# Performance work log

Hardware: AMD Instinct MI355X
Metric: run time of the kernel (lower is better)

## Reference

```python
import math
import jax, jax.numpy as jnp
import numpy as np

N = 65536   # total nodes across episodes
H = 512     # hidden size
B = 4096    # number of episodes / decoding items
M = 32      # max neighbors (padded ragged valid_actions)


def setup_inputs() -> dict:
    key = jax.random.key(0)
    ks = jax.random.split(key, 9)
    s = 1.0 / math.sqrt(H)
    return {
        "h_static": jax.random.normal(ks[0], (N, H), jnp.float32),
        "h_dynamic": jax.random.normal(ks[1], (N, H), jnp.float32),
        "Ws_kvl": jax.random.normal(ks[2], (H, 3 * H), jnp.float32) * s,
        "Wd_kvl": jax.random.normal(ks[3], (H, 3 * H), jnp.float32) * s,
        "Wq": jax.random.normal(ks[4], (H, H), jnp.float32) * s,
        "batch": jax.random.randint(ks[5], (N,), 0, B, jnp.int32),
        "current_nodes": jax.random.randint(ks[6], (B,), 0, N),
        "neigh_idx": jax.random.randint(ks[7], (B, M), 0, N),
        "lengths": jax.random.randint(ks[8], (B,), 0, M + 1),
    }


def reference(h_static, h_dynamic, Ws_kvl, Wd_kvl, Wq, batch, current_nodes, neigh_idx, lengths):
    # precompute(): static KVL projection (full 3H GEMM then chunk, as in torch)
    kvl_s = h_static @ Ws_kvl            # [N, 3H]
    K_s = kvl_s[:, :H]
    # forward_batch(): dynamic projection
    kvl_d = h_dynamic @ Wd_kvl           # [N, 3H]
    K_d = kvl_d[:, :H]
    K = K_s + K_d                        # [N, H]  (V is computed but unused for outputs)
    q = (h_static[current_nodes] + h_dynamic[current_nodes]) @ Wq  # [B, H]

    # padded ragged neighbor attention (replaces the Python loop over B)
    Kn = K[neigh_idx]                                        # [B, M, H]
    compat = jnp.einsum('bmh,bh->bm', Kn, q) / math.sqrt(H)  # [B, M]
    mask = jnp.arange(M)[None, :] < lengths[:, None]         # [B, M]
    NEG = jnp.float32(-1e9)
    logits = jnp.where(mask, compat, NEG)

    # categorical sampling via Gumbel-max (Categorical(logits).sample())
    u = jax.random.uniform(jax.random.key(1), (B, M), jnp.float32, 1e-8, 1.0)
    g = -jnp.log(-jnp.log(u))
    idx = jnp.argmax(logits + g, axis=-1)                    # [B]

    logp = jax.nn.log_softmax(logits, axis=-1)               # [B, M]
    lp = jnp.take_along_axis(logp, idx[:, None], axis=1)[:, 0]
    actions = jnp.take_along_axis(neigh_idx, idx[:, None], axis=1)[:, 0]

    # empty neighbor list -> stay at current node, log_prob 0 (matches torch branch)
    nonempty = lengths > 0
    actions = jnp.where(nonempty, actions, current_nodes)
    lp = jnp.where(nonempty, lp, jnp.float32(0.0))
    return actions, lp
```

## Files before the change

kernel.cpp:

```cpp
#include <hip/hip_runtime.h>
#include <cstdint>
#include <cstddef>

#define HDIM 512
#define NM 32
#define NBATCH 4096
#define NNODE 65536
#define CAP 16

typedef float v4f __attribute__((ext_vector_type(4)));

__device__ __forceinline__ unsigned rotl32(unsigned x, unsigned d) {
  return (x << d) | (x >> (32u - d));
}

__device__ __forceinline__ void threefry2x32(unsigned& x0, unsigned& x1) {
  const unsigned ks0 = 0u, ks1 = 1u, ks2 = 0x1BD11BDBu;
  x0 += ks0; x1 += ks1;
#define TF_RND(r) { x0 += x1; x1 = rotl32(x1, (r)); x1 ^= x0; }
  TF_RND(13) TF_RND(15) TF_RND(26) TF_RND(6)
  x0 += ks1; x1 += ks2 + 1u;
  TF_RND(17) TF_RND(29) TF_RND(16) TF_RND(24)
  x0 += ks2; x1 += ks0 + 2u;
  TF_RND(13) TF_RND(15) TF_RND(26) TF_RND(6)
  x0 += ks0; x1 += ks1 + 3u;
  TF_RND(17) TF_RND(29) TF_RND(16) TF_RND(24)
  x0 += ks1; x1 += ks2 + 4u;
  TF_RND(13) TF_RND(15) TF_RND(26) TF_RND(6)
  x0 += ks2; x1 += ks0 + 5u;
#undef TF_RND
}

__global__ __launch_bounds__(256) void zero_cnt(int* __restrict__ cnt,
                                                int* __restrict__ ovf_cnt) {
  const int t = blockIdx.x * 256 + threadIdx.x;
  ((int4*)cnt)[t] = make_int4(0, 0, 0, 0);
  if (t == 0) *ovf_cnt = 0;
}

__global__ __launch_bounds__(256) void gemm_b1(const float* __restrict__ Ws,
                                               const float* __restrict__ Wd,
                                               const float* __restrict__ Wq,
                                               float* __restrict__ M2T) {
  constexpr int BK = 16, LDT = 68;
  __shared__ float Ast[BK][LDT];
  __shared__ float Bst[BK][LDT];
  const int tid = threadIdx.x;
  const int row0 = blockIdx.y * 64;
  const int col0 = blockIdx.x * 64;
  const float* Abase = (row0 < 512) ? Ws : Wd;
  const int arow0 = (row0 < 512) ? row0 : row0 - 512;
  const int tx = tid & 15, ty = tid >> 4;
  const int lr = tid >> 2, lc = (tid & 3) * 4;
  float acc[4][4] = {};
  for (int k0 = 0; k0 < 512; k0 += BK) {
    float4 va = *(const float4*)(Abase + (size_t)(arow0 + lr) * 1536 + k0 + lc);
    float4 vb = *(const float4*)(Wq + (size_t)(col0 + lr) * 512 + k0 + lc);
    Ast[lc + 0][lr] = va.x; Ast[lc + 1][lr] = va.y;
    Ast[lc + 2][lr] = va.z; Ast[lc + 3][lr] = va.w;
    Bst[lc + 0][lr] = vb.x; Bst[lc + 1][lr] = vb.y;
    Bst[lc + 2][lr] = vb.z; Bst[lc + 3][lr] = vb.w;
    __syncthreads();
#pragma unroll
    for (int k = 0; k < BK; ++k) {
      float4 a4 = *(const float4*)&Ast[k][ty * 4];
      float4 b4 = *(const float4*)&Bst[k][tx * 4];
      float a[4] = {a4.x, a4.y, a4.z, a4.w};
      float bb[4] = {b4.x, b4.y, b4.z, b4.w};
#pragma unroll
      for (int i = 0; i < 4; ++i)
#pragma unroll
        for (int j = 0; j < 4; ++j) acc[i][j] += a[i] * bb[j];
    }
    __syncthreads();
  }
#pragma unroll
  for (int i = 0; i < 4; ++i) {
    float4 o;
    o.x = acc[i][0]; o.y = acc[i][1]; o.z = acc[i][2]; o.w = acc[i][3];
    *(float4*)(M2T + (size_t)(row0 + ty * 4 + i) * 512 + col0 + tx * 4) = o;
  }
}

__global__ __launch_bounds__(256) void gemm_v(const float* __restrict__ hs,
                                              const float* __restrict__ hd,
                                              const int* __restrict__ cur,
                                              const float* __restrict__ Bm,
                                              float* __restrict__ C) {
  constexpr int BK = 32, LDT = 68;
  __shared__ float Ast[BK][LDT];
  __shared__ float Bst[BK][LDT];
  const int tid = threadIdx.x;
  const int row0 = blockIdx.y * 64;
  const int col0 = blockIdx.x * 64;
  const int tx = tid & 15, ty = tid >> 4;
  const int lr = tid >> 3;
  const int lc = (tid & 7) * 4;
  const size_t n0 = (size_t)cur[row0 + lr] * HDIM;
  const size_t n1 = (size_t)cur[row0 + lr + 32] * HDIM;
  float acc[4][4] = {};
  for (int k0 = 0; k0 < 512; k0 += BK) {
    const float4 s0 = *(const float4*)(hs + n0 + k0 + lc);
    const float4 d0 = *(const float4*)(hd + n0 + k0 + lc);
    const float4 s1 = *(const float4*)(hs + n1 + k0 + lc);
    const float4 d1 = *(const float4*)(hd + n1 + k0 + lc);
    const float4 vb0 = *(const float4*)(Bm + (size_t)(col0 + lr) * 512 + k0 + lc);
    const float4 vb1 = *(const float4*)(Bm + (size_t)(col0 + lr + 32) * 512 + k0 + lc);
    Ast[lc + 0][lr] = s0.x + d0.x; Ast[lc + 1][lr] = s0.y + d0.y;
    Ast[lc + 2][lr] = s0.z + d0.z; Ast[lc + 3][lr] = s0.w + d0.w;
    Ast[lc + 0][lr + 32] = s1.x + d1.x; Ast[lc + 1][lr + 32] = s1.y + d1.y;
    Ast[lc + 2][lr + 32] = s1.z + d1.z; Ast[lc + 3][lr + 32] = s1.w + d1.w;
    Bst[lc + 0][lr] = vb0.x; Bst[lc + 1][lr] = vb0.y;
    Bst[lc + 2][lr] = vb0.z; Bst[lc + 3][lr] = vb0.w;
    Bst[lc + 0][lr + 32] = vb1.x; Bst[lc + 1][lr + 32] = vb1.y;
    Bst[lc + 2][lr + 32] = vb1.z; Bst[lc + 3][lr + 32] = vb1.w;
    __syncthreads();
#pragma unroll
    for (int k = 0; k < BK; ++k) {
      const float4 a4 = *(const float4*)&Ast[k][ty * 4];
      const float4 b4 = *(const float4*)&Bst[k][tx * 4];
      const float a[4] = {a4.x, a4.y, a4.z, a4.w};
      const float bb[4] = {b4.x, b4.y, b4.z, b4.w};
#pragma unroll
      for (int i = 0; i < 4; ++i)
#pragma unroll
        for (int j = 0; j < 4; ++j) acc[i][j] += a[i] * bb[j];
    }
    __syncthreads();
  }
#pragma unroll
  for (int i = 0; i < 4; ++i) {
    float4 o;
    o.x = acc[i][0]; o.y = acc[i][1]; o.z = acc[i][2]; o.w = acc[i][3];
    *(float4*)(C + (size_t)(row0 + ty * 4 + i) * 1024 + col0 + tx * 4) = o;
  }
}

__global__ __launch_bounds__(256) void build_index(
    const int* __restrict__ neigh, const int* __restrict__ lens,
    int* __restrict__ cnt, int* __restrict__ bucket,
    int* __restrict__ ovf_cnt, int* __restrict__ ovf_list) {
  const int t = blockIdx.x * 256 + threadIdx.x;
  const int b = t >> 5, m = t & 31;
  if (m < lens[b]) {
    const int n = neigh[t];
    const int slot = atomicAdd(&cnt[n], 1);
    if (slot < CAP) bucket[n * CAP + slot] = t;
    else { const int o = atomicAdd(ovf_cnt, 1); ovf_list[o] = t; }
  }
}

__global__ __launch_bounds__(256) void stream_compat(
    const float* __restrict__ hs, const float* __restrict__ hd,
    const float* __restrict__ V, const int* __restrict__ cnt,
    const int* __restrict__ bucket, const int* __restrict__ ovf_cnt,
    const int* __restrict__ ovf_list, const int* __restrict__ neigh,
    float* __restrict__ compat) {
  const int n = blockIdx.x * 4 + (threadIdx.x >> 6);
  const int lane = threadIdx.x & 63;
  const int c = cnt[n];
  if (c != 0) {
    const v4f* a4 = (const v4f*)(hs + (size_t)n * HDIM);
    const v4f* c4 = (const v4f*)(hd + (size_t)n * HDIM);
    const v4f a0 = __builtin_nontemporal_load(a4 + lane * 2);
    const v4f a1 = __builtin_nontemporal_load(a4 + lane * 2 + 1);
    const v4f b0 = __builtin_nontemporal_load(c4 + lane * 2);
    const v4f b1 = __builtin_nontemporal_load(c4 + lane * 2 + 1);
    const int cc = (c < CAP) ? c : CAP;
    for (int e = 0; e < cc; ++e) {
      const int t = bucket[n * CAP + e];
      const int b = t >> 5;
      const float4* vrow = (const float4*)(V + (size_t)b * (2 * HDIM));
      const float4 w0 = vrow[lane * 2], w1 = vrow[lane * 2 + 1];
      const float4 u0 = vrow[128 + lane * 2], u1 = vrow[128 + lane * 2 + 1];
      float acc = a0.x * w0.x + a0.y * w0.y + a0.z * w0.z + a0.w * w0.w
                + a1.x * w1.x + a1.y * w1.y + a1.z * w1.z + a1.w * w1.w
                + b0.x * u0.x + b0.y * u0.y + b0.z * u0.z + b0.w * u0.w
                + b1.x * u1.x + b1.y * u1.y + b1.z * u1.z + b1.w * u1.w;
#pragma unroll
      for (int off = 32; off >= 1; off >>= 1) acc += __shfl_xor(acc, off);
      if (lane == 0) compat[t] = acc;
    }
  }
  if (blockIdx.x < 32) {
    const int nw = *ovf_cnt;
    for (int e = blockIdx.x * 4 + (threadIdx.x >> 6); e < nw; e += 128) {
      const int t = ovf_list[e];
      const int b = t >> 5;
      const int nn = neigh[t];
      const float4* a4 = (const float4*)(hs + (size_t)nn * HDIM);
      const float4* c4 = (const float4*)(hd + (size_t)nn * HDIM);
      const float4 a0 = a4[lane * 2], a1 = a4[lane * 2 + 1];
      const float4 b0 = c4[lane * 2], b1 = c4[lane * 2 + 1];
      const float4* vrow = (const float4*)(V + (size_t)b * (2 * HDIM));
      const float4 w0 = vrow[lane * 2], w1 = vrow[lane * 2 + 1];
      const float4 u0 = vrow[128 + lane * 2], u1 = vrow[128 + lane * 2 + 1];
      float acc = a0.x * w0.x + a0.y * w0.y + a0.z * w0.z + a0.w * w0.w
                + a1.x * w1.x + a1.y * w1.y + a1.z * w1.z + a1.w * w1.w
                + b0.x * u0.x + b0.y * u0.y + b0.z * u0.z + b0.w * u0.w
                + b1.x * u1.x + b1.y * u1.y + b1.z * u1.z + b1.w * u1.w;
#pragma unroll
      for (int off = 32; off >= 1; off >>= 1) acc += __shfl_xor(acc, off);
      if (lane == 0) compat[t] = acc;
    }
  }
}

__global__ __launch_bounds__(256) void finalize_kernel(
    const float* __restrict__ compat, const int* __restrict__ neigh,
    const int* __restrict__ lengths, const int* __restrict__ cur,
    float* __restrict__ out) {
  const int b = blockIdx.x * 4 + (threadIdx.x >> 6);
  const int tid = threadIdx.x & 63;
  const int len = lengths[b];
  const bool valid = tid < NM;
  const float NEGMAX = -3.402823466e38f;
  float logit = NEGMAX;
  if (valid) {
    const float cm = compat[b * NM + tid] / 22.62741699796952f;
    logit = (tid < len) ? cm : -1e9f;
  }
  float z = NEGMAX;
  int zi = 1 << 20;
  if (valid) {
    const unsigned i_lo = (unsigned)b * 32u + (unsigned)tid;
    unsigned x0 = 0u;
    unsigned x1 = i_lo;
    threefry2x32(x0, x1);
    const unsigned bits = x0 ^ x1;
    const float fu = __uint_as_float((bits >> 9) | 0x3f800000u) - 1.0f;
    const float uu = fmaxf(1e-8f, fu + 1e-8f);
    const float g = -logf(-logf(uu));
    z = logit + g;
    zi = tid;
  }
#pragma unroll
  for (int off = 32; off >= 1; off >>= 1) {
    const float oz = __shfl_xor(z, off);
    const int oi = __shfl_xor(zi, off);
    if (oz > z || (oz == z && oi < zi)) { z = oz; zi = oi; }
  }
  float ml = logit;
#pragma unroll
  for (int off = 32; off >= 1; off >>= 1) ml = fmaxf(ml, __shfl_xor(ml, off));
  float ex = valid ? expf(logit - ml) : 0.f;
#pragma unroll
  for (int off = 32; off >= 1; off >>= 1) ex += __shfl_xor(ex, off);
  const float lsel = __shfl(logit, zi);
  if (tid == 0) {
    float lp = lsel - ml - logf(ex);
    int act = neigh[b * NM + zi];
    if (len <= 0) { act = cur[b]; lp = 0.f; }
    out[b] = (float)act;
    out[NBATCH + b] = lp;
  }
}

extern "C" void kernel_launch(void* const* d_in, const int* in_sizes, int n_in,
                              void* d_out, int out_size, void* d_ws, size_t ws_size,
                              hipStream_t stream) {
  const float* hs = (const float*)d_in[0];
  const float* hd = (const float*)d_in[1];
  const float* Ws = (const float*)d_in[2];
  const float* Wd = (const float*)d_in[3];
  const float* Wq = (const float*)d_in[4];
  const int* cur = (const int*)d_in[6];
  const int* neigh = (const int*)d_in[7];
  const int* lens = (const int*)d_in[8];
  float* out = (float*)d_out;

  char* ws = (char*)d_ws;
  size_t off = 0;
  int* cnt = (int*)(ws + off);        off += (size_t)NNODE * 4;
  int* ovf_cnt = (int*)(ws + off);    off += 256;
  int* bucket = (int*)(ws + off);     off += (size_t)NNODE * CAP * 4;
  int* ovf_list = (int*)(ws + off);   off += (size_t)NBATCH * NM * 4;
  float* compat = (float*)(ws + off); off += (size_t)NBATCH * NM * 4;
  float* M2T = (float*)(ws + off);    off += (size_t)1024 * 512 * 4;
  float* V = (float*)(ws + off);      off += (size_t)NBATCH * 2 * HDIM * 4;

  hipLaunchKernelGGL(zero_cnt, dim3(64), dim3(256), 0, stream, cnt, ovf_cnt);
  hipLaunchKernelGGL(build_index, dim3(NBATCH * NM / 256), dim3(256), 0, stream,
                     neigh, lens, cnt, bucket, ovf_cnt, ovf_list);
  hipLaunchKernelGGL(gemm_b1, dim3(8, 16), dim3(256), 0, stream, Ws, Wd, Wq, M2T);
  hipLaunchKernelGGL(gemm_v, dim3(16, 64), dim3(256), 0, stream, hs, hd, cur, M2T, V);
  hipLaunchKernelGGL(stream_compat, dim3(NNODE / 4), dim3(256), 0, stream,
                     hs, hd, V, cnt, bucket, ovf_cnt, ovf_list, neigh, compat);
  hipLaunchKernelGGL(finalize_kernel, dim3(NBATCH / 4), dim3(256), 0, stream,
                     compat, neigh, lens, cur, out);
}
```

Before: 168.1 us.

## Fuse weight GEMM with index build and double-buffer the query GEMM

Folds the neighbor-bucket index build into the small weight-product GEMM launch as extra blocks, which removes one kernel launch and lets the two independent jobs run concurrently. The query-side GEMM now double-buffers its shared-memory tiles, prefetching the next K slice into registers during compute and dropping one barrier per iteration. It also swizzles the block-to-tile mapping to change cache locality. In exchange, the GEMM uses twice the LDS, which may lower occupancy.

```diff
diff --git a/kernel.cpp b/kernel.cpp
--- a/kernel.cpp
+++ b/kernel.cpp
@@ -38,16 +38,30 @@
   if (t == 0) *ovf_cnt = 0;
 }
 
-__global__ __launch_bounds__(256) void gemm_b1(const float* __restrict__ Ws,
-                                               const float* __restrict__ Wd,
-                                               const float* __restrict__ Wq,
-                                               float* __restrict__ M2T) {
+__global__ __launch_bounds__(256) void b1_and_index(
+    const float* __restrict__ Ws, const float* __restrict__ Wd,
+    const float* __restrict__ Wq, float* __restrict__ M2T,
+    const int* __restrict__ neigh, const int* __restrict__ lens,
+    int* __restrict__ cnt, int* __restrict__ bucket,
+    int* __restrict__ ovf_cnt, int* __restrict__ ovf_list) {
   constexpr int BK = 16, LDT = 68;
   __shared__ float Ast[BK][LDT];
   __shared__ float Bst[BK][LDT];
+  const int bid = blockIdx.x;
   const int tid = threadIdx.x;
-  const int row0 = blockIdx.y * 64;
-  const int col0 = blockIdx.x * 64;
+  if (bid >= 128) {
+    const int t = (bid - 128) * 256 + tid;
+    const int b = t >> 5, m = t & 31;
+    if (m < lens[b]) {
+      const int n = neigh[t];
+      const int slot = atomicAdd(&cnt[n], 1);
+      if (slot < CAP) bucket[n * CAP + slot] = t;
+      else { const int o = atomicAdd(ovf_cnt, 1); ovf_list[o] = t; }
+    }
+    return;
+  }
+  const int row0 = (bid >> 3) * 64;
+  const int col0 = (bid & 7) * 64;
   const float* Abase = (row0 < 512) ? Ws : Wd;
   const int arow0 = (row0 < 512) ? row0 : row0 - 512;
   const int tx = tid & 15, ty = tid >> 4;
@@ -88,37 +102,53 @@
                                               const float* __restrict__ Bm,
                                               float* __restrict__ C) {
   constexpr int BK = 32, LDT = 68;
-  __shared__ float Ast[BK][LDT];
-  __shared__ float Bst[BK][LDT];
+  __shared__ float Ast[2][BK][LDT];
+  __shared__ float Bst[2][BK][LDT];
   const int tid = threadIdx.x;
-  const int row0 = blockIdx.y * 64;
-  const int col0 = blockIdx.x * 64;
+  const int swz = (blockIdx.x & 7) * 128 + (blockIdx.x >> 3);
+  const int row0 = (swz >> 4) * 64;
+  const int col0 = (swz & 15) * 64;
   const int tx = tid & 15, ty = tid >> 4;
   const int lr = tid >> 3;
   const int lc = (tid & 7) * 4;
-  const size_t n0 = (size_t)cur[row0 + lr] * HDIM;
-  const size_t n1 = (size_t)cur[row0 + lr + 32] * HDIM;
+  const size_t n0 = (size_t)cur[row0 + lr] * HDIM + lc;
+  const size_t n1 = (size_t)cur[row0 + lr + 32] * HDIM + lc;
+  const float* bp0 = Bm + (size_t)(col0 + lr) * 512 + lc;
+  const float* bp1 = Bm + (size_t)(col0 + lr + 32) * 512 + lc;
+
+  float4 s0 = *(const float4*)(hs + n0);
+  float4 d0 = *(const float4*)(hd + n0);
+  float4 s1 = *(const float4*)(hs + n1);
+  float4 d1 = *(const float4*)(hd + n1);
+  float4 vb0 = *(const float4*)(bp0);
+  float4 vb1 = *(const float4*)(bp1);
+
   float acc[4][4] = {};
-  for (int k0 = 0; k0 < 512; k0 += BK) {
-    const float4 s0 = *(const float4*)(hs + n0 + k0 + lc);
-    const float4 d0 = *(const float4*)(hd + n0 + k0 + lc);
-    const float4 s1 = *(const float4*)(hs + n1 + k0 + lc);
-    const float4 d1 = *(const float4*)(hd + n1 + k0 + lc);
-    const float4 vb0 = *(const float4*)(Bm + (size_t)(col0 + lr) * 512 + k0 + lc);
-    const float4 vb1 = *(const float4*)(Bm + (size_t)(col0 + lr + 32) * 512 + k0 + lc);
-    Ast[lc + 0][lr] = s0.x + d0.x; Ast[lc + 1][lr] = s0.y + d0.y;
-    Ast[lc + 2][lr] = s0.z + d0.z; Ast[lc + 3][lr] = s0.w + d0.w;
-    Ast[lc + 0][lr + 32] = s1.x + d1.x; Ast[lc + 1][lr + 32] = s1.y + d1.y;
-    Ast[lc + 2][lr + 32] = s1.z + d1.z; Ast[lc + 3][lr + 32] = s1.w + d1.w;
-    Bst[lc + 0][lr] = vb0.x; Bst[lc + 1][lr] = vb0.y;
-    Bst[lc + 2][lr] = vb0.z; Bst[lc + 3][lr] = vb0.w;
-    Bst[lc + 0][lr + 32] = vb1.x; Bst[lc + 1][lr + 32] = vb1.y;
-    Bst[lc + 2][lr + 32] = vb1.z; Bst[lc + 3][lr + 32] = vb1.w;
+  int cb = 0;
+#pragma unroll 1
+  for (int t = 0; t < 16; ++t) {
+    Ast[cb][lc + 0][lr] = s0.x + d0.x; Ast[cb][lc + 1][lr] = s0.y + d0.y;
+    Ast[cb][lc + 2][lr] = s0.z + d0.z; Ast[cb][lc + 3][lr] = s0.w + d0.w;
+    Ast[cb][lc + 0][lr + 32] = s1.x + d1.x; Ast[cb][lc + 1][lr + 32] = s1.y + d1.y;
+    Ast[cb][lc + 2][lr + 32] = s1.z + d1.z; Ast[cb][lc + 3][lr + 32] = s1.w + d1.w;
+    Bst[cb][lc + 0][lr] = vb0.x; Bst[cb][lc + 1][lr] = vb0.y;
+    Bst[cb][lc + 2][lr] = vb0.z; Bst[cb][lc + 3][lr] = vb0.w;
+    Bst[cb][lc + 0][lr + 32] = vb1.x; Bst[cb][lc + 1][lr + 32] = vb1.y;
+    Bst[cb][lc + 2][lr + 32] = vb1.z; Bst[cb][lc + 3][lr + 32] = vb1.w;
     __syncthreads();
+    if (t < 15) {
+      const int k0 = (t + 1) * BK;
+      s0 = *(const float4*)(hs + n0 + k0);
+      d0 = *(const float4*)(hd + n0 + k0);
+      s1 = *(const float4*)(hs + n1 + k0);
+      d1 = *(const float4*)(hd + n1 + k0);
+      vb0 = *(const float4*)(bp0 + k0);
+      vb1 = *(const float4*)(bp1 + k0);
+    }
 #pragma unroll
     for (int k = 0; k < BK; ++k) {
-      const float4 a4 = *(const float4*)&Ast[k][ty * 4];
-      const float4 b4 = *(const float4*)&Bst[k][tx * 4];
+      const float4 a4 = *(const float4*)&Ast[cb][k][ty * 4];
+      const float4 b4 = *(const float4*)&Bst[cb][k][tx * 4];
       const float a[4] = {a4.x, a4.y, a4.z, a4.w};
       const float bb[4] = {b4.x, b4.y, b4.z, b4.w};
 #pragma unroll
@@ -126,27 +156,13 @@
 #pragma unroll
         for (int j = 0; j < 4; ++j) acc[i][j] += a[i] * bb[j];
     }
-    __syncthreads();
+    cb ^= 1;
   }
 #pragma unroll
   for (int i = 0; i < 4; ++i) {
     float4 o;
     o.x = acc[i][0]; o.y = acc[i][1]; o.z = acc[i][2]; o.w = acc[i][3];
     *(float4*)(C + (size_t)(row0 + ty * 4 + i) * 1024 + col0 + tx * 4) = o;
-  }
-}
-
-__global__ __launch_bounds__(256) void build_index(
-    const int* __restrict__ neigh, const int* __restrict__ lens,
-    int* __restrict__ cnt, int* __restrict__ bucket,
-    int* __restrict__ ovf_cnt, int* __restrict__ ovf_list) {
-  const int t = blockIdx.x * 256 + threadIdx.x;
-  const int b = t >> 5, m = t & 31;
-  if (m < lens[b]) {
-    const int n = neigh[t];
-    const int slot = atomicAdd(&cnt[n], 1);
-    if (slot < CAP) bucket[n * CAP + slot] = t;
-    else { const int o = atomicAdd(ovf_cnt, 1); ovf_list[o] = t; }
   }
 }
 
@@ -280,10 +296,9 @@
   float* V = (float*)(ws + off);      off += (size_t)NBATCH * 2 * HDIM * 4;
 
   hipLaunchKernelGGL(zero_cnt, dim3(64), dim3(256), 0, stream, cnt, ovf_cnt);
-  hipLaunchKernelGGL(build_index, dim3(NBATCH * NM / 256), dim3(256), 0, stream,
-                     neigh, lens, cnt, bucket, ovf_cnt, ovf_list);
-  hipLaunchKernelGGL(gemm_b1, dim3(8, 16), dim3(256), 0, stream, Ws, Wd, Wq, M2T);
-  hipLaunchKernelGGL(gemm_v, dim3(16, 64), dim3(256), 0, stream, hs, hd, cur, M2T, V);
+  hipLaunchKernelGGL(b1_and_index, dim3(128 + NBATCH * NM / 256), dim3(256), 0, stream,
+                     Ws, Wd, Wq, M2T, neigh, lens, cnt, bucket, ovf_cnt, ovf_list);
+  hipLaunchKernelGGL(gemm_v, dim3(1024), dim3(256), 0, stream, hs, hd, cur, M2T, V);
   hipLaunchKernelGGL(stream_compat, dim3(NNODE / 4), dim3(256), 0, stream,
                      hs, hd, V, cnt, bucket, ovf_cnt, ovf_list, neigh, compat);
   hipLaunchKernelGGL(finalize_kernel, dim3(NBATCH / 4), dim3(256), 0, stream,
```

Result: no change. 166.9 us (-0.7%).
